# Optimization experiments

Hardware: AMD Instinct MI355X
Metric: run time of the kernel (lower is better)

Reference implementation:

```python
import jax, jax.numpy as jnp
import numpy as np

EPS = 1e-8  # F.cosine_similarity default eps


def setup_inputs() -> dict:
    key = jax.random.key(0)
    k1, = jax.random.split(key, 1)
    x = jax.random.normal(k1, (16384, 512), dtype=jnp.float32)
    w = jnp.float32(10.0)   # init_w parameter
    b = jnp.float32(-5.0)   # init_b parameter
    return {"x": x, "w": w, "b": b}


def reference(x, w, b):
    # x: [2N, D] interleaved (anchor, positive) embeddings
    anchor = x[0::2]    # [N, D]
    positive = x[1::2]  # [N, D]
    N = anchor.shape[0]

    # cosine similarity matrix: cos[i, j] = <pos_i, anc_j> / max(|pos_i||anc_j|, eps)
    # (normalize + GEMM instead of the O(N*D*N) broadcast)
    dots = jnp.einsum('id,jd->ij', positive, anchor)          # [N, N]
    pn = jnp.linalg.norm(positive, axis=1)                    # [N]
    an = jnp.linalg.norm(anchor, axis=1)                      # [N]
    denom = jnp.maximum(pn[:, None] * an[None, :], EPS)
    cos_sim = dots / denom

    logits = cos_sim * w + b                                  # [N, N]
    labels = jnp.arange(N)

    # CrossEntropyLoss (mean reduction)
    logp = jax.nn.log_softmax(logits, axis=1)
    nloss = -jnp.mean(logp[jnp.arange(N), labels])
    return nloss
```

## Files before the change

### kernel.cpp

```cpp
#include <hip/hip_runtime.h>
#include <hip/hip_bf16.h>

typedef __attribute__((ext_vector_type(8))) short short8;
typedef __attribute__((ext_vector_type(4))) float f32x4;

#define D 512
#define NT 8

typedef const __attribute__((address_space(1))) void gvoid;
typedef __attribute__((address_space(3))) void lvoid;

__device__ inline unsigned pack2f(float lo, float hi) {
    __hip_bfloat162 v = __float22bfloat162_rn(make_float2(lo, hi));
    union { __hip_bfloat162 h; unsigned u; } cv;
    cv.h = v;
    return cv.u;
}

__device__ inline int4 pack8f(const float4& v0, const float4& v1, float sc) {
    int4 r;
    r.x = (int)pack2f(v0.x * sc, v0.y * sc);
    r.y = (int)pack2f(v0.z * sc, v0.w * sc);
    r.z = (int)pack2f(v1.x * sc, v1.y * sc);
    r.w = (int)pack2f(v1.z * sc, v1.w * sc);
    return r;
}

__global__ __launch_bounds__(512) void norm_kernel(
    const float* __restrict__ x,
    float* __restrict__ diag, float* __restrict__ sumexp,
    __hip_bfloat16* __restrict__ Pn, __hip_bfloat16* __restrict__ An)
{
    const int t = threadIdx.x;
    const int i = blockIdx.x * 8 + (t >> 6);
    const int lane = t & 63;
    const float4* ap = (const float4*)(x + (size_t)(2 * i) * D);
    const float4* pp = (const float4*)(x + (size_t)(2 * i + 1) * D);
    float4 a0 = ap[lane * 2], a1 = ap[lane * 2 + 1];
    float4 p0 = pp[lane * 2], p1 = pp[lane * 2 + 1];
    float ssa = a0.x*a0.x + a0.y*a0.y + a0.z*a0.z + a0.w*a0.w
              + a1.x*a1.x + a1.y*a1.y + a1.z*a1.z + a1.w*a1.w;
    float ssp = p0.x*p0.x + p0.y*p0.y + p0.z*p0.z + p0.w*p0.w
              + p1.x*p1.x + p1.y*p1.y + p1.z*p1.z + p1.w*p1.w;
    float dt  = p0.x*a0.x + p0.y*a0.y + p0.z*a0.z + p0.w*a0.w
              + p1.x*a1.x + p1.y*a1.y + p1.z*a1.z + p1.w*a1.w;
#pragma unroll
    for (int m = 1; m < 64; m <<= 1) {
        ssa += __shfl_xor(ssa, m);
        ssp += __shfl_xor(ssp, m);
        dt  += __shfl_xor(dt, m);
    }
    float an = sqrtf(ssa), pn = sqrtf(ssp);
    float ia = 1.0f / fmaxf(an, 1e-30f);
    float ip = 1.0f / fmaxf(pn, 1e-30f);
    if (lane == 0) {
        diag[i] = dt / fmaxf(pn * an, 1e-8f);
        sumexp[i] = 0.0f;
    }
    int4 wp_, wa_;
    wp_ = pack8f(make_float4(p0.x,p0.y,p0.z,p0.w), make_float4(p1.x,p1.y,p1.z,p1.w), ip);
    wa_ = pack8f(make_float4(a0.x,a0.y,a0.z,a0.w), make_float4(a1.x,a1.y,a1.z,a1.w), ia);
    ((int4*)(Pn + (size_t)i * D))[lane] = wp_;
    ((int4*)(An + (size_t)i * D))[lane] = wa_;
}

__global__ __launch_bounds__(512, 2) void gemm_lse_256(
    const __hip_bfloat16* __restrict__ Pn, const __hip_bfloat16* __restrict__ An,
    const float* __restrict__ wp, float* __restrict__ sumexp, int nbx)
{
    __shared__ __align__(16) unsigned char lds[131072];

    const int t = threadIdx.x;
    const int lane = t & 63, w = t >> 6;
    const int wm = w >> 2, wn = w & 3;
    const int l15 = lane & 15, lhi = lane >> 4;
    const int swz = (l15 & 7) << 4;
    const int kb0 = lhi * 16, kb1 = 64 + lhi * 16;

    const int nwg = nbx * nbx;
    const int cpx = nwg >> 3;
    const int bid = blockIdx.x;
    const int wgid = (bid & 7) * cpx + (bid >> 3);
    const int brow = (wgid / nbx) * 256;
    const int bcol = (wgid % nbx) * 256;

    const float wv = *wp;
    const float s = fabsf(wv);

    const int o_0 = t * 16, o_1 = t * 16 + 8192;
    const int rl0 = o_0 >> 7, rl1 = o_1 >> 7;
    const int ss0 = ((o_0 >> 4) & 7) ^ (rl0 & 7);
    const int ss1 = ((o_1 >> 4) & 7) ^ (rl1 & 7);

    const __hip_bfloat16* g0[4];
    const __hip_bfloat16* g1[4];
    g0[0] = Pn + (size_t)(brow +   0 + rl0) * D + ss0 * 8;
    g1[0] = Pn + (size_t)(brow +   0 + rl1) * D + ss1 * 8;
    g0[1] = An + (size_t)(bcol +   0 + rl0) * D + ss0 * 8;
    g1[1] = An + (size_t)(bcol +   0 + rl1) * D + ss1 * 8;
    g0[2] = An + (size_t)(bcol + 128 + rl0) * D + ss0 * 8;
    g1[2] = An + (size_t)(bcol + 128 + rl1) * D + ss1 * 8;
    g0[3] = Pn + (size_t)(brow + 128 + rl0) * D + ss0 * 8;
    g1[3] = Pn + (size_t)(brow + 128 + rl1) * D + ss1 * 8;

    const int sbase[4] = { 0, 65536, 65536 + 16384, 16384 };

#define STAGE(H, DN, KOFF) do {                                                            \
        unsigned char* _d = lds + sbase[H] + (DN) * 32768;                                 \
        __builtin_amdgcn_global_load_lds((gvoid*)(g0[H] + (KOFF)), (lvoid*)(_d + o_0), 16, 0, 0); \
        __builtin_amdgcn_global_load_lds((gvoid*)(g1[H] + (KOFF)), (lvoid*)(_d + o_1), 16, 0, 0); \
    } while (0)

#define RDA(OFF) do {                                                                      \
        _Pragma("unroll")                                                                  \
        for (int mi = 0; mi < 4; ++mi) {                                                   \
            a[0][mi] = *(const short8*)(lAc + (OFF) + mi * 2048 + (kb0 ^ swz));            \
            a[1][mi] = *(const short8*)(lAc + (OFF) + mi * 2048 + (kb1 ^ swz));            \
        }                                                                                  \
    } while (0)

#define RDB(BB, OFF) do {                                                                  \
        _Pragma("unroll")                                                                  \
        for (int nf = 0; nf < 2; ++nf) {                                                   \
            BB[0][nf] = *(const short8*)(lBc + (OFF) + nf * 2048 + (kb0 ^ swz));           \
            BB[1][nf] = *(const short8*)(lBc + (OFF) + nf * 2048 + (kb1 ^ swz));           \
        }                                                                                  \
    } while (0)

#define MF(MB, NB, BB) do {                                                                \
        __builtin_amdgcn_s_setprio(1);                                                     \
        _Pragma("unroll")                                                                  \
        for (int ks = 0; ks < 2; ++ks) {                                                   \
            _Pragma("unroll")                                                              \
            for (int mi = 0; mi < 4; ++mi) {                                               \
                _Pragma("unroll")                                                          \
                for (int nf = 0; nf < 2; ++nf)                                             \
                    acc[(MB) + mi][(NB) + nf] = __builtin_amdgcn_mfma_f32_16x16x32_bf16(   \
                        a[ks][mi], BB[ks][nf], acc[(MB) + mi][(NB) + nf], 0, 0, 0);        \
            }                                                                              \
        }                                                                                  \
        __builtin_amdgcn_s_setprio(0);                                                     \
    } while (0)

#define LGKM0 do { asm volatile("s_waitcnt lgkmcnt(0)" ::: "memory");                      \
                   __builtin_amdgcn_sched_barrier(0); } while (0)

    f32x4 acc[8][4];
#pragma unroll
    for (int mi = 0; mi < 8; ++mi)
#pragma unroll
        for (int ni = 0; ni < 4; ++ni)
#pragma unroll
            for (int j = 0; j < 4; ++j) acc[mi][ni][j] = 0.0f;

    STAGE(0, 0, 0);
    STAGE(1, 0, 0);
    STAGE(2, 0, 0);
    STAGE(3, 0, 0);
    asm volatile("s_waitcnt vmcnt(4)" ::: "memory");
    __builtin_amdgcn_s_barrier();

    short8 a[2][4], b0[2][2], b1[2][2];
    const unsigned char* lAc;
    const unsigned char* lBc;

    for (int tn = 0; tn < NT - 1; ++tn) {
        const int c = tn & 1, dn = c ^ 1;
        const int koff = (tn + 1) * 64;
        lAc = lds + c * 32768 + wm * 8192 + l15 * 128;
        lBc = lds + 65536 + c * 32768 + wn * 4096 + l15 * 128;

        RDA(0);
        RDB(b0, 0);
        STAGE(0, dn, koff);
        __builtin_amdgcn_s_barrier();
        LGKM0;
        MF(0, 0, b0);
        asm volatile("s_waitcnt vmcnt(4)" ::: "memory");
        __builtin_amdgcn_s_barrier();

        RDB(b1, 16384);
        STAGE(1, dn, koff);
        __builtin_amdgcn_s_barrier();
        LGKM0;
        MF(0, 2, b1);
        asm volatile("s_waitcnt vmcnt(4)" ::: "memory");
        __builtin_amdgcn_s_barrier();

        RDA(16384);
        STAGE(2, dn, koff);
        __builtin_amdgcn_s_barrier();
        LGKM0;
        MF(4, 2, b1);
        __builtin_amdgcn_s_barrier();

        STAGE(3, dn, koff);
        __builtin_amdgcn_s_barrier();
        MF(4, 0, b0);
        asm volatile("s_waitcnt vmcnt(4)" ::: "memory");
        __builtin_amdgcn_s_barrier();
    }

    {
        lAc = lds + 32768 + wm * 8192 + l15 * 128;
        lBc = lds + 65536 + 32768 + wn * 4096 + l15 * 128;

        RDA(0);
        RDB(b0, 0);
        __builtin_amdgcn_s_barrier();
        LGKM0;
        MF(0, 0, b0);
        asm volatile("s_waitcnt vmcnt(2)" ::: "memory");
        __builtin_amdgcn_s_barrier();

        RDB(b1, 16384);
        __builtin_amdgcn_s_barrier();
        LGKM0;
        MF(0, 2, b1);
        asm volatile("s_waitcnt vmcnt(0)" ::: "memory");
        __builtin_amdgcn_s_barrier();

        RDA(16384);
        __builtin_amdgcn_s_barrier();
        LGKM0;
        MF(4, 2, b1);
        __builtin_amdgcn_s_barrier();

        MF(4, 0, b0);
    }

#undef STAGE
#undef RDA
#undef RDB
#undef MF
#undef LGKM0

#pragma unroll
    for (int mi = 0; mi < 8; ++mi) {
#pragma unroll
        for (int j = 0; j < 4; ++j) {
            float v = 0.0f;
#pragma unroll
            for (int ni = 0; ni < 4; ++ni)
                v += __expf(acc[mi][ni][j] * wv - s);
            v += __shfl_xor(v, 1);
            v += __shfl_xor(v, 2);
            v += __shfl_xor(v, 4);
            v += __shfl_xor(v, 8);
            if (l15 == 0) {
                int row = brow + (mi >> 2) * 128 + wm * 64 + (mi & 3) * 16 + lhi * 4 + j;
                atomicAdd(&sumexp[row], v);
            }
        }
    }
}

__global__ __launch_bounds__(256, 2) void gemm_lse_small(
    const float* __restrict__ x,
    const float* __restrict__ pinv, const float* __restrict__ ainv,
    const float* __restrict__ wp, float* __restrict__ sumexp, int N)
{
    __shared__ __align__(16) unsigned char lds[81920];
    unsigned char* As = lds;
    unsigned char* Bs = lds + 65536;

    const int t = threadIdx.x;
    const int rb = blockIdx.y, cs = blockIdx.x;
    const int lane = t & 63, w = t >> 6;
    const int wr = w >> 1, wc = w & 1;
    const int l15 = lane & 15, lhi = lane >> 4;

    const int colsPer = N >> 3;
    const int CT = colsPer / 64;
    const int Q = CT * (D / 64);

    {
        int r = t >> 2;
        int kq = (t & 3) << 7;
        int grow = rb * 64 + r;
        const float4* src = (const float4*)(x + (size_t)(2 * grow + 1) * D);
        float sc = pinv[grow];
#pragma unroll
        for (int i2 = 0; i2 < 16; ++i2) {
            int k0 = kq + i2 * 8;
            float4 v0 = src[k0 >> 2], v1 = src[(k0 >> 2) + 1];
            *(int4*)(As + r * 1024 + ((k0 * 2) ^ ((r & 7) << 4))) = pack8f(v0, v1, sc);
        }
    }

    const int cl = t >> 2;
    const int kq = (t & 3) << 4;

    auto loadB = [&](int q, int4& oa, int4& ob) {
        int ct = q >> 3, kc = q & 7;
        int c = cs * colsPer + ct * 64 + cl;
        int k = kc * 64 + kq;
        const float4* src = (const float4*)(x + (size_t)(2 * c) * D + k);
        float sc = ainv[c];
        float4 v0 = src[0], v1 = src[1], v2 = src[2], v3 = src[3];
        oa = pack8f(v0, v1, sc);
        ob = pack8f(v2, v3, sc);
    };
    auto writeB = [&](int buf, const int4& oa, const int4& ob) {
        unsigned char* bb = Bs + buf * 8192 + cl * 128;
        int kb0 = kq * 2;
        *(int4*)(bb + (kb0 ^ ((cl & 7) << 4))) = oa;
        *(int4*)(bb + ((kb0 + 16) ^ ((cl & 7) << 4))) = ob;
    };

    const float wv = *wp;
    const float s = fabsf(wv);

    int4 ba, bb2;
    loadB(0, ba, bb2);
    __syncthreads();
    writeB(0, ba, bb2);
    __syncthreads();

    f32x4 acc[2][2];
    float rs[2][4];
#pragma unroll
    for (int mi = 0; mi < 2; ++mi) {
#pragma unroll
        for (int j = 0; j < 4; ++j) rs[mi][j] = 0.0f;
#pragma unroll
        for (int ni = 0; ni < 2; ++ni)
#pragma unroll
            for (int j = 0; j < 4; ++j) acc[mi][ni][j] = 0.0f;
    }

    for (int q = 0; q < Q; ++q) {
        const int kc = q & 7;
        const bool more = (q + 1 < Q);
        if (more) loadB(q + 1, ba, bb2);
        const unsigned char* Bp = Bs + (q & 1) * 8192;
#pragma unroll
        for (int ks = 0; ks < 2; ++ks) {
            int ka = kc * 64 + ks * 32 + lhi * 8;
            int ra0 = wr * 32 + l15, ra1 = ra0 + 16;
            short8 a0 = *(const short8*)(As + ra0 * 1024 + ((ka * 2) ^ ((ra0 & 7) << 4)));
            short8 a1 = *(const short8*)(As + ra1 * 1024 + ((ka * 2) ^ ((ra1 & 7) << 4)));
            int kb = ks * 32 + lhi * 8;
            int c0 = wc * 32 + l15, c1 = c0 + 16;
            short8 b0 = *(const short8*)(Bp + c0 * 128 + ((kb * 2) ^ ((c0 & 7) << 4)));
            short8 b1 = *(const short8*)(Bp + c1 * 128 + ((kb * 2) ^ ((c1 & 7) << 4)));
            acc[0][0] = __builtin_amdgcn_mfma_f32_16x16x32_bf16(a0, b0, acc[0][0], 0, 0, 0);
            acc[0][1] = __builtin_amdgcn_mfma_f32_16x16x32_bf16(a0, b1, acc[0][1], 0, 0, 0);
            acc[1][0] = __builtin_amdgcn_mfma_f32_16x16x32_bf16(a1, b0, acc[1][0], 0, 0, 0);
            acc[1][1] = __builtin_amdgcn_mfma_f32_16x16x32_bf16(a1, b1, acc[1][1], 0, 0, 0);
        }
        if (kc == 7) {
#pragma unroll
            for (int mi = 0; mi < 2; ++mi)
#pragma unroll
                for (int ni = 0; ni < 2; ++ni)
#pragma unroll
                    for (int j = 0; j < 4; ++j) {
                        rs[mi][j] += __expf(acc[mi][ni][j] * wv - s);
                        acc[mi][ni][j] = 0.0f;
                    }
        }
        if (more) {
            __syncthreads();
            writeB((q + 1) & 1, ba, bb2);
            __syncthreads();
        }
    }

#pragma unroll
    for (int mi = 0; mi < 2; ++mi)
#pragma unroll
        for (int j = 0; j < 4; ++j) {
            float v = rs[mi][j];
            v += __shfl_xor(v, 1);
            v += __shfl_xor(v, 2);
            v += __shfl_xor(v, 4);
            v += __shfl_xor(v, 8);
            if (l15 == 0) {
                int row = rb * 64 + wr * 32 + mi * 16 + lhi * 4 + j;
                atomicAdd(&sumexp[row], v);
            }
        }
}

__global__ __launch_bounds__(512) void norm_small(
    const float* __restrict__ x,
    float* __restrict__ pinv, float* __restrict__ ainv,
    float* __restrict__ diag, float* __restrict__ sumexp)
{
    const int t = threadIdx.x;
    const int i = blockIdx.x * 8 + (t >> 6);
    const int lane = t & 63;
    const float4* ap = (const float4*)(x + (size_t)(2 * i) * D);
    const float4* pp = (const float4*)(x + (size_t)(2 * i + 1) * D);
    float4 a0 = ap[lane * 2], a1 = ap[lane * 2 + 1];
    float4 p0 = pp[lane * 2], p1 = pp[lane * 2 + 1];
    float ssa = a0.x*a0.x + a0.y*a0.y + a0.z*a0.z + a0.w*a0.w
              + a1.x*a1.x + a1.y*a1.y + a1.z*a1.z + a1.w*a1.w;
    float ssp = p0.x*p0.x + p0.y*p0.y + p0.z*p0.z + p0.w*p0.w
              + p1.x*p1.x + p1.y*p1.y + p1.z*p1.z + p1.w*p1.w;
    float dt  = p0.x*a0.x + p0.y*a0.y + p0.z*a0.z + p0.w*a0.w
              + p1.x*a1.x + p1.y*a1.y + p1.z*a1.z + p1.w*a1.w;
#pragma unroll
    for (int m = 1; m < 64; m <<= 1) {
        ssa += __shfl_xor(ssa, m);
        ssp += __shfl_xor(ssp, m);
        dt  += __shfl_xor(dt, m);
    }
    float an = sqrtf(ssa), pn = sqrtf(ssp);
    if (lane == 0) {
        ainv[i] = 1.0f / fmaxf(an, 1e-30f);
        pinv[i] = 1.0f / fmaxf(pn, 1e-30f);
        diag[i] = dt / fmaxf(pn * an, 1e-8f);
        sumexp[i] = 0.0f;
    }
}

__global__ __launch_bounds__(1024) void finalize_kernel(
    const float* __restrict__ sumexp, const float* __restrict__ diag,
    const float* __restrict__ wp, float* __restrict__ out, int N)
{
    const int t = threadIdx.x;
    const float w = *wp;
    const float s = fabsf(w);
    float acc = 0.0f;
    for (int i = t; i < N; i += 1024)
        acc += s + logf(sumexp[i]) - w * diag[i];
#pragma unroll
    for (int m = 1; m < 64; m <<= 1) acc += __shfl_xor(acc, m);
    __shared__ float red[16];
    if ((t & 63) == 0) red[t >> 6] = acc;
    __syncthreads();
    if (t == 0) {
        float v = 0.0f;
#pragma unroll
        for (int i = 0; i < 16; ++i) v += red[i];
        out[0] = v / (float)N;
    }
}

extern "C" void kernel_launch(void* const* d_in, const int* in_sizes, int n_in,
                              void* d_out, int out_size, void* d_ws, size_t ws_size,
                              hipStream_t stream) {
    const float* x  = (const float*)d_in[0];
    const float* wp = (const float*)d_in[1];

    const int N = in_sizes[0] / (2 * D);

    char* ws = (char*)d_ws;
    size_t nf = (size_t)N * 4;
    float* pinv   = (float*)(ws);
    float* ainv   = (float*)(ws + nf);
    float* diag   = (float*)(ws + 2 * nf);
    float* sumexp = (float*)(ws + 3 * nf);
    size_t base = (4 * nf + 255) & ~(size_t)255;
    __hip_bfloat16* Pn = (__hip_bfloat16*)(ws + base);
    __hip_bfloat16* An = (__hip_bfloat16*)(ws + base + (size_t)N * D * 2);
    const bool cached = ws_size >= base + (size_t)N * D * 4;

    if (cached) {
        norm_kernel<<<N / 8, 512, 0, stream>>>(x, diag, sumexp, Pn, An);
        const int nbx = N / 256;
        gemm_lse_256<<<nbx * nbx, 512, 0, stream>>>(Pn, An, wp, sumexp, nbx);
    } else {
        norm_small<<<N / 8, 512, 0, stream>>>(x, pinv, ainv, diag, sumexp);
        dim3 grid(8, N / 64);
        gemm_lse_small<<<grid, 256, 0, stream>>>(x, pinv, ainv, wp, sumexp, N);
    }

    finalize_kernel<<<1, 1024, 0, stream>>>(sumexp, diag, wp, (float*)d_out, N);
}
```

Measured before the change: 241.8 us.

## Switch normalized GEMM to FP8 e4m3 MFMA with halved LDS tiles

The normalization kernel now quantizes the unit-normalized rows (scaled by 16) to FP8 e4m3 with a software rounding routine, in place of bf16. The 256x256 GEMM-LSE kernel uses the fp8 16x16x32 MFMA, stages half as many bytes per tile with one global_load_lds per thread and a new 4-way swizzle, and halves LDS so four blocks can be resident per CU. The exponent scale folds in the 1/256 factor. This aims to cut matrix-core time and memory/LDS traffic, at the cost of lower precision in the cosine similarities, which w=10 amplifies in the logits.

```diff
diff --git a/kernel.cpp b/kernel.cpp
--- a/kernel.cpp
+++ b/kernel.cpp
@@ -9,6 +9,16 @@
 
 typedef const __attribute__((address_space(1))) void gvoid;
 typedef __attribute__((address_space(3))) void lvoid;
+
+__device__ inline unsigned f32_to_e4m3(float x) {
+    union { float f; unsigned u; } c; c.f = x;
+    unsigned s  = (c.u >> 24) & 0x80u;
+    unsigned ab = c.u & 0x7FFFFFFFu;
+    if (ab < 0x3C800000u) return s;
+    unsigned r = ab + 0x0007FFFFu + ((ab >> 20) & 1u);
+    unsigned e = (r >> 23) - 120u;
+    return s | (e << 3) | ((r >> 20) & 7u);
+}
 
 __device__ inline unsigned pack2f(float lo, float hi) {
     __hip_bfloat162 v = __float22bfloat162_rn(make_float2(lo, hi));
@@ -26,10 +36,10 @@
     return r;
 }
 
-__global__ __launch_bounds__(512) void norm_kernel(
+__global__ __launch_bounds__(512) void norm_kernel8(
     const float* __restrict__ x,
     float* __restrict__ diag, float* __restrict__ sumexp,
-    __hip_bfloat16* __restrict__ Pn, __hip_bfloat16* __restrict__ An)
+    unsigned char* __restrict__ Pn, unsigned char* __restrict__ An)
 {
     const int t = threadIdx.x;
     const int i = blockIdx.x * 8 + (t >> 6);
@@ -57,25 +67,34 @@
         diag[i] = dt / fmaxf(pn * an, 1e-8f);
         sumexp[i] = 0.0f;
     }
-    int4 wp_, wa_;
-    wp_ = pack8f(make_float4(p0.x,p0.y,p0.z,p0.w), make_float4(p1.x,p1.y,p1.z,p1.w), ip);
-    wa_ = pack8f(make_float4(a0.x,a0.y,a0.z,a0.w), make_float4(a1.x,a1.y,a1.z,a1.w), ia);
-    ((int4*)(Pn + (size_t)i * D))[lane] = wp_;
-    ((int4*)(An + (size_t)i * D))[lane] = wa_;
-}
-
-__global__ __launch_bounds__(512, 2) void gemm_lse_256(
-    const __hip_bfloat16* __restrict__ Pn, const __hip_bfloat16* __restrict__ An,
+    const float fp = ip * 16.0f, fa = ia * 16.0f;
+    uint2 wp8, wa8;
+    wp8.x = f32_to_e4m3(p0.x*fp) | (f32_to_e4m3(p0.y*fp) << 8) |
+            (f32_to_e4m3(p0.z*fp) << 16) | (f32_to_e4m3(p0.w*fp) << 24);
+    wp8.y = f32_to_e4m3(p1.x*fp) | (f32_to_e4m3(p1.y*fp) << 8) |
+            (f32_to_e4m3(p1.z*fp) << 16) | (f32_to_e4m3(p1.w*fp) << 24);
+    wa8.x = f32_to_e4m3(a0.x*fa) | (f32_to_e4m3(a0.y*fa) << 8) |
+            (f32_to_e4m3(a0.z*fa) << 16) | (f32_to_e4m3(a0.w*fa) << 24);
+    wa8.y = f32_to_e4m3(a1.x*fa) | (f32_to_e4m3(a1.y*fa) << 8) |
+            (f32_to_e4m3(a1.z*fa) << 16) | (f32_to_e4m3(a1.w*fa) << 24);
+    ((uint2*)(Pn + (size_t)i * D))[lane] = wp8;
+    ((uint2*)(An + (size_t)i * D))[lane] = wa8;
+}
+
+__global__ __launch_bounds__(512, 4) void gemm_lse_256f8(
+    const unsigned char* __restrict__ Pn, const unsigned char* __restrict__ An,
     const float* __restrict__ wp, float* __restrict__ sumexp, int nbx)
 {
-    __shared__ __align__(16) unsigned char lds[131072];
+    __shared__ __align__(16) unsigned char lds[65536];
 
     const int t = threadIdx.x;
     const int lane = t & 63, w = t >> 6;
     const int wm = w >> 2, wn = w & 3;
     const int l15 = lane & 15, lhi = lane >> 4;
-    const int swz = (l15 & 7) << 4;
-    const int kb0 = lhi * 16, kb1 = 64 + lhi * 16;
+    const int rsw = l15 & 3;
+
+    const int ksw0 = (((0 * 2 + (lhi >> 1)) ^ rsw) << 4) + ((lhi & 1) << 3);
+    const int ksw1 = (((1 * 2 + (lhi >> 1)) ^ rsw) << 4) + ((lhi & 1) << 3);
 
     const int nwg = nbx * nbx;
     const int cpx = nwg >> 3;
@@ -86,44 +105,38 @@
 
     const float wv = *wp;
     const float s = fabsf(wv);
-
-    const int o_0 = t * 16, o_1 = t * 16 + 8192;
-    const int rl0 = o_0 >> 7, rl1 = o_1 >> 7;
-    const int ss0 = ((o_0 >> 4) & 7) ^ (rl0 & 7);
-    const int ss1 = ((o_1 >> 4) & 7) ^ (rl1 & 7);
-
-    const __hip_bfloat16* g0[4];
-    const __hip_bfloat16* g1[4];
-    g0[0] = Pn + (size_t)(brow +   0 + rl0) * D + ss0 * 8;
-    g1[0] = Pn + (size_t)(brow +   0 + rl1) * D + ss1 * 8;
-    g0[1] = An + (size_t)(bcol +   0 + rl0) * D + ss0 * 8;
-    g1[1] = An + (size_t)(bcol +   0 + rl1) * D + ss1 * 8;
-    g0[2] = An + (size_t)(bcol + 128 + rl0) * D + ss0 * 8;
-    g1[2] = An + (size_t)(bcol + 128 + rl1) * D + ss1 * 8;
-    g0[3] = Pn + (size_t)(brow + 128 + rl0) * D + ss0 * 8;
-    g1[3] = Pn + (size_t)(brow + 128 + rl1) * D + ss1 * 8;
-
-    const int sbase[4] = { 0, 65536, 65536 + 16384, 16384 };
+    const float wsc = wv * (1.0f / 256.0f);
+
+    const int o_0 = t * 16;
+    const int rl = t >> 2;
+    const int ss = (t & 3) ^ (rl & 3);
+
+    const unsigned char* g0[4];
+    g0[0] = Pn + (size_t)(brow +   0 + rl) * D + ss * 16;
+    g0[1] = An + (size_t)(bcol +   0 + rl) * D + ss * 16;
+    g0[2] = An + (size_t)(bcol + 128 + rl) * D + ss * 16;
+    g0[3] = Pn + (size_t)(brow + 128 + rl) * D + ss * 16;
+
+    const int sbase[4] = { 0, 32768, 32768 + 8192, 8192 };
 
 #define STAGE(H, DN, KOFF) do {                                                            \
-        unsigned char* _d = lds + sbase[H] + (DN) * 32768;                                 \
+        unsigned char* _d = lds + sbase[H] + (DN) * 16384;                                 \
         __builtin_amdgcn_global_load_lds((gvoid*)(g0[H] + (KOFF)), (lvoid*)(_d + o_0), 16, 0, 0); \
-        __builtin_amdgcn_global_load_lds((gvoid*)(g1[H] + (KOFF)), (lvoid*)(_d + o_1), 16, 0, 0); \
     } while (0)
 
-#define RDA(OFF) do {                                                                      \
+#define RDA(H) do {                                                                        \
         _Pragma("unroll")                                                                  \
         for (int mi = 0; mi < 4; ++mi) {                                                   \
-            a[0][mi] = *(const short8*)(lAc + (OFF) + mi * 2048 + (kb0 ^ swz));            \
-            a[1][mi] = *(const short8*)(lAc + (OFF) + mi * 2048 + (kb1 ^ swz));            \
+            a[0][mi] = *(const long*)(lAc + (H) * 8192 + mi * 1024 + ksw0);                \
+            a[1][mi] = *(const long*)(lAc + (H) * 8192 + mi * 1024 + ksw1);                \
         }                                                                                  \
     } while (0)
 
-#define RDB(BB, OFF) do {                                                                  \
+#define RDB(BB, H) do {                                                                    \
         _Pragma("unroll")                                                                  \
         for (int nf = 0; nf < 2; ++nf) {                                                   \
-            BB[0][nf] = *(const short8*)(lBc + (OFF) + nf * 2048 + (kb0 ^ swz));           \
-            BB[1][nf] = *(const short8*)(lBc + (OFF) + nf * 2048 + (kb1 ^ swz));           \
+            BB[0][nf] = *(const long*)(lBc + (H) * 8192 + nf * 1024 + ksw0);               \
+            BB[1][nf] = *(const long*)(lBc + (H) * 8192 + nf * 1024 + ksw1);               \
         }                                                                                  \
     } while (0)
 
@@ -135,7 +148,7 @@
             for (int mi = 0; mi < 4; ++mi) {                                               \
                 _Pragma("unroll")                                                          \
                 for (int nf = 0; nf < 2; ++nf)                                             \
-                    acc[(MB) + mi][(NB) + nf] = __builtin_amdgcn_mfma_f32_16x16x32_bf16(   \
+                    acc[(MB) + mi][(NB) + nf] = __builtin_amdgcn_mfma_f32_16x16x32_fp8_fp8(\
                         a[ks][mi], BB[ks][nf], acc[(MB) + mi][(NB) + nf], 0, 0, 0);        \
             }                                                                              \
         }                                                                                  \
@@ -157,18 +170,18 @@
     STAGE(1, 0, 0);
     STAGE(2, 0, 0);
     STAGE(3, 0, 0);
-    asm volatile("s_waitcnt vmcnt(4)" ::: "memory");
+    asm volatile("s_waitcnt vmcnt(2)" ::: "memory");
     __builtin_amdgcn_s_barrier();
 
-    short8 a[2][4], b0[2][2], b1[2][2];
+    long a[2][4], b0[2][2], b1[2][2];
     const unsigned char* lAc;
     const unsigned char* lBc;
 
     for (int tn = 0; tn < NT - 1; ++tn) {
         const int c = tn & 1, dn = c ^ 1;
         const int koff = (tn + 1) * 64;
-        lAc = lds + c * 32768 + wm * 8192 + l15 * 128;
-        lBc = lds + 65536 + c * 32768 + wn * 4096 + l15 * 128;
+        lAc = lds + c * 16384 + (wm * 64 + l15) * 64;
+        lBc = lds + 32768 + c * 16384 + (wn * 32 + l15) * 64;
 
         RDA(0);
         RDB(b0, 0);
@@ -176,18 +189,18 @@
         __builtin_amdgcn_s_barrier();
         LGKM0;
         MF(0, 0, b0);
-        asm volatile("s_waitcnt vmcnt(4)" ::: "memory");
-        __builtin_amdgcn_s_barrier();
-
-        RDB(b1, 16384);
+        asm volatile("s_waitcnt vmcnt(2)" ::: "memory");
+        __builtin_amdgcn_s_barrier();
+
+        RDB(b1, 1);
         STAGE(1, dn, koff);
         __builtin_amdgcn_s_barrier();
         LGKM0;
         MF(0, 2, b1);
-        asm volatile("s_waitcnt vmcnt(4)" ::: "memory");
-        __builtin_amdgcn_s_barrier();
-
-        RDA(16384);
+        asm volatile("s_waitcnt vmcnt(2)" ::: "memory");
+        __builtin_amdgcn_s_barrier();
+
+        RDA(1);
         STAGE(2, dn, koff);
         __builtin_amdgcn_s_barrier();
         LGKM0;
@@ -197,30 +210,30 @@
         STAGE(3, dn, koff);
         __builtin_amdgcn_s_barrier();
         MF(4, 0, b0);
-        asm volatile("s_waitcnt vmcnt(4)" ::: "memory");
+        asm volatile("s_waitcnt vmcnt(2)" ::: "memory");
         __builtin_amdgcn_s_barrier();
     }
 
     {
-        lAc = lds + 32768 + wm * 8192 + l15 * 128;
-        lBc = lds + 65536 + 32768 + wn * 4096 + l15 * 128;
+        lAc = lds + 16384 + (wm * 64 + l15) * 64;
+        lBc = lds + 32768 + 16384 + (wn * 32 + l15) * 64;
 
         RDA(0);
         RDB(b0, 0);
         __builtin_amdgcn_s_barrier();
         LGKM0;
         MF(0, 0, b0);
-        asm volatile("s_waitcnt vmcnt(2)" ::: "memory");
-        __builtin_amdgcn_s_barrier();
-
-        RDB(b1, 16384);
+        asm volatile("s_waitcnt vmcnt(1)" ::: "memory");
+        __builtin_amdgcn_s_barrier();
+
+        RDB(b1, 1);
         __builtin_amdgcn_s_barrier();
         LGKM0;
         MF(0, 2, b1);
         asm volatile("s_waitcnt vmcnt(0)" ::: "memory");
         __builtin_amdgcn_s_barrier();
 
-        RDA(16384);
+        RDA(1);
         __builtin_amdgcn_s_barrier();
         LGKM0;
         MF(4, 2, b1);
@@ -242,7 +255,7 @@
             float v = 0.0f;
 #pragma unroll
             for (int ni = 0; ni < 4; ++ni)
-                v += __expf(acc[mi][ni][j] * wv - s);
+                v += __expf(acc[mi][ni][j] * wsc - s);
             v += __shfl_xor(v, 1);
             v += __shfl_xor(v, 2);
             v += __shfl_xor(v, 4);
@@ -454,14 +467,14 @@
     float* diag   = (float*)(ws + 2 * nf);
     float* sumexp = (float*)(ws + 3 * nf);
     size_t base = (4 * nf + 255) & ~(size_t)255;
-    __hip_bfloat16* Pn = (__hip_bfloat16*)(ws + base);
-    __hip_bfloat16* An = (__hip_bfloat16*)(ws + base + (size_t)N * D * 2);
-    const bool cached = ws_size >= base + (size_t)N * D * 4;
+    unsigned char* Pn8 = (unsigned char*)(ws + base);
+    unsigned char* An8 = (unsigned char*)(ws + base + (size_t)N * D);
+    const bool cached = ws_size >= base + (size_t)N * D * 2;
 
     if (cached) {
-        norm_kernel<<<N / 8, 512, 0, stream>>>(x, diag, sumexp, Pn, An);
+        norm_kernel8<<<N / 8, 512, 0, stream>>>(x, diag, sumexp, Pn8, An8);
         const int nbx = N / 256;
-        gemm_lse_256<<<nbx * nbx, 512, 0, stream>>>(Pn, An, wp, sumexp, nbx);
+        gemm_lse_256f8<<<nbx * nbx, 512, 0, stream>>>(Pn8, An8, wp, sumexp, nbx);
     } else {
         norm_small<<<N / 8, 512, 0, stream>>>(x, pinv, ainv, diag, sumexp);
         dim3 grid(8, N / 64);
```

New measurement: 512.8 us. 112% more time.
